# Performance work log

Measured on AMD Instinct MI355X. Metric: run time of the kernel, lower is better.

## Reference

```python
import jax, jax.numpy as jnp
import numpy as np

NODE_IN, EDGE_IN, HID, L = 16, 8, 128, 4
N_NODES, N_EDGES = 50000, 600000
EPS = 1e-5


def setup_inputs() -> dict:
    key = jax.random.key(0)
    ks = jax.random.split(key, 20)
    def lin(k, fan_in, fan_out):
        b = 1.0 / np.sqrt(fan_in)
        kw, kb = jax.random.split(k)
        return (jax.random.uniform(kw, (fan_in, fan_out), jnp.float32, -b, b),
                jax.random.uniform(kb, (fan_out,), jnp.float32, -b, b))
    x = jax.random.normal(ks[0], (N_NODES, NODE_IN), jnp.float32)
    edge_index = jax.random.randint(ks[1], (2, N_EDGES), 0, N_NODES, jnp.int64)
    edge_attr = jax.random.normal(ks[2], (N_EDGES, EDGE_IN), jnp.float32)
    node_w, node_b = lin(ks[3], NODE_IN, HID)
    edge_w, edge_b = lin(ks[4], EDGE_IN, HID)
    lnode_w, lnode_b, ledge_w, ledge_b, adm_w, adm_b = [], [], [], [], [], []
    for l in range(L):
        w, b = lin(ks[5 + 3 * l], HID, HID); lnode_w.append(w); lnode_b.append(b)
        w, b = lin(ks[6 + 3 * l], HID, HID); ledge_w.append(w); ledge_b.append(b)
        w, b = lin(ks[7 + 3 * l], HID, 1); adm_w.append(w); adm_b.append(b)
    return {
        "x": x, "edge_index": edge_index, "edge_attr": edge_attr,
        "node_w": node_w, "node_b": node_b, "edge_w": edge_w, "edge_b": edge_b,
        "lnode_w": jnp.stack(lnode_w), "lnode_b": jnp.stack(lnode_b),
        "ledge_w": jnp.stack(ledge_w), "ledge_b": jnp.stack(ledge_b),
        "adm_w": jnp.stack(adm_w), "adm_b": jnp.stack(adm_b),
        "gamma": jnp.ones((L, HID), jnp.float32),
        "beta": jnp.zeros((L, HID), jnp.float32),
    }


def reference(x, edge_index, edge_attr, node_w, node_b, edge_w, edge_b,
              lnode_w, lnode_b, ledge_w, ledge_b, adm_w, adm_b, gamma, beta):
    N = x.shape[0]
    src, dst = edge_index[0], edge_index[1]
    h = x @ node_w + node_b              # [N, HID]
    ea = edge_attr @ edge_w + edge_b     # [E, HID]
    for l in range(lnode_w.shape[0]):
        hn = h @ lnode_w[l] + lnode_b[l]                         # lin_node
        y_mag = jax.nn.sigmoid(ea @ adm_w[l] + adm_b[l])         # [E, 1] admittance gate
        e = ea @ ledge_w[l] + ledge_b[l]                         # lin_edge
        msg = y_mag * (hn[src] + e)                              # gated message [E, HID]
        agg = jax.ops.segment_sum(msg, dst, num_segments=N)      # scatter-add
        mu = jnp.mean(agg, axis=-1, keepdims=True)
        var = jnp.mean((agg - mu) ** 2, axis=-1, keepdims=True)
        xn = (agg - mu) * jax.lax.rsqrt(var + EPS) * gamma[l] + beta[l]
        h = h + jax.nn.relu(xn)          # dropout is identity in eval mode
    return h
```

## Files before the change

kernel.cpp:

```cpp
#include <hip/hip_runtime.h>
#include <math.h>

#define N_NODES 50000
#define N_EDGES 600000
#define HID 128
#define NLAYERS 4
#define NODE_IN 16
#define EDGE_IN 8
#define LN_EPS 1e-5f
#define SCAN_BLOCKS ((N_NODES + 255) / 256)
#define ENC_BASE (4864 + NLAYERS * HID * HID)
#define PRE_TOTAL (ENC_BASE + N_NODES * HID)

typedef short bf16x8 __attribute__((ext_vector_type(8)));
typedef float f32x4 __attribute__((ext_vector_type(4)));

__device__ __forceinline__ float b2f(unsigned short u) {
    union { unsigned int i; float f; } v; v.i = ((unsigned int)u) << 16; return v.f;
}
__device__ __forceinline__ unsigned short f2b(float x) {
    union { float f; unsigned int i; } v; v.f = x;
    unsigned int b = v.i + 0x7FFFu + ((v.i >> 16) & 1u);
    return (unsigned short)(b >> 16);
}

__global__ void detect_i64(const int* ei, int* flag) {
    __shared__ int nz;
    if (threadIdx.x == 0) nz = 0;
    __syncthreads();
    int acc = 0;
    for (int i = threadIdx.x; i < 1024; i += blockDim.x)
        if (ei[2 * i + 1] != 0) acc = 1;
    if (acc) atomicOr(&nz, 1);
    __syncthreads();
    if (threadIdx.x == 0) *flag = (nz == 0) ? 1 : 0;
}

__device__ __forceinline__ int edge_src(const void* ei, int f, int e) {
    if (f) return (int)((const long long*)ei)[e];
    return ((const int*)ei)[e];
}
__device__ __forceinline__ int edge_dst(const void* ei, int f, int e) {
    if (f) return (int)((const long long*)ei)[N_EDGES + e];
    return ((const int*)ei)[N_EDGES + e];
}

__global__ void hist_k(const void* ei, const int* flag, int* cursor) {
    int e = blockIdx.x * blockDim.x + threadIdx.x;
    if (e >= N_EDGES) return;
    int f = *flag;
    atomicAdd(&cursor[edge_dst(ei, f, e)], 1);
}

__global__ void scan1_k(const int* __restrict__ cursor, int* __restrict__ locex,
                        int* __restrict__ partials) {
    __shared__ int sd[256];
    int t = threadIdx.x, i = blockIdx.x * 256 + t;
    int v = (i < N_NODES) ? cursor[i] : 0;
    sd[t] = v;
    __syncthreads();
    for (int off = 1; off < 256; off <<= 1) {
        int x = (t >= off) ? sd[t - off] : 0;
        __syncthreads();
        sd[t] += x;
        __syncthreads();
    }
    if (i < N_NODES) locex[i] = sd[t] - v;
    if (t == 255) partials[blockIdx.x] = sd[255];
}

__global__ void scan2_k(int* partials) {
    __shared__ int sd[256];
    int t = threadIdx.x;
    int v = (t < SCAN_BLOCKS) ? partials[t] : 0;
    sd[t] = v;
    __syncthreads();
    for (int off = 1; off < 256; off <<= 1) {
        int x = (t >= off) ? sd[t - off] : 0;
        __syncthreads();
        sd[t] += x;
        __syncthreads();
    }
    if (t < SCAN_BLOCKS) partials[t] = sd[t] - v;
    if (t == 255) partials[SCAN_BLOCKS] = sd[255];
}

__global__ void scan3_k(int* __restrict__ row_ptr, int* __restrict__ cursor,
                        const int* __restrict__ partials) {
    int i = blockIdx.x * 256 + threadIdx.x;
    if (i < N_NODES) {
        int r = row_ptr[i] + partials[blockIdx.x];
        row_ptr[i] = r;
        cursor[i] = r;
    }
    if (i == N_NODES) row_ptr[N_NODES] = partials[SCAN_BLOCKS];
}

__global__ void place_k(const void* ei, const int* flag, int* cursor,
                        int* sorted_src, int* sorted_eid) {
    int e = blockIdx.x * blockDim.x + threadIdx.x;
    if (e >= N_EDGES) return;
    int f = *flag;
    int s = edge_src(ei, f, e);
    int d = edge_dst(ei, f, e);
    int pos = atomicAdd(&cursor[d], 1);
    sorted_src[pos] = s;
    sorted_eid[pos] = e;
}

__global__ void precomp_all_k(const float* __restrict__ edge_w, const float* __restrict__ edge_b,
                              const float* __restrict__ ledge_w, const float* __restrict__ ledge_b,
                              const float* __restrict__ lnode_b, const float* __restrict__ lnode_w,
                              const float* __restrict__ adm_w, const float* __restrict__ adm_b,
                              const float* __restrict__ x, const float* __restrict__ node_w,
                              const float* __restrict__ node_b,
                              float* __restrict__ M, float* __restrict__ cb,
                              float* __restrict__ v, float* __restrict__ cgate,
                              unsigned short* __restrict__ Wt16,
                              unsigned short* __restrict__ h16) {
    int t = blockIdx.x * 256 + threadIdx.x;
    if (t < 4096) {
        int l = t >> 10, k = (t >> 7) & 7, ch = t & 127;
        const float* lw = ledge_w + (size_t)l * HID * HID;
        float a = 0.f;
        for (int j = 0; j < HID; ++j) a += edge_w[k * HID + j] * lw[j * HID + ch];
        M[t] = a;
    } else if (t < 4608) {
        int u = t - 4096;
        int l = u >> 7, ch = u & 127;
        const float* lw = ledge_w + (size_t)l * HID * HID;
        float a = ledge_b[l * HID + ch] + lnode_b[l * HID + ch];
        for (int j = 0; j < HID; ++j) a += edge_b[j] * lw[j * HID + ch];
        cb[u] = a;
    } else if (t < 4640) {
        int u = t - 4608;
        int l = u >> 3, k = u & 7;
        float a = 0.f;
        for (int j = 0; j < HID; ++j) a += edge_w[k * HID + j] * adm_w[l * HID + j];
        v[u] = a;
    } else if (t < 4644) {
        int l = t - 4640;
        float a = adm_b[l];
        for (int j = 0; j < HID; ++j) a += edge_b[j] * adm_w[l * HID + j];
        cgate[l] = a;
    } else if (t >= 4864 && t < ENC_BASE) {
        int idx = t - 4864;
        int l = idx >> 14, r = idx & 16383, n = r >> 7, k = r & 127;
        Wt16[idx] = f2b(lnode_w[(size_t)l * HID * HID + k * HID + n]);
    } else if (t >= ENC_BASE && t < PRE_TOTAL) {
        int idx = t - ENC_BASE;
        int n = idx >> 7, c = idx & 127;
        float acc = node_b[c];
#pragma unroll
        for (int k = 0; k < NODE_IN; ++k) acc += x[n * NODE_IN + k] * node_w[k * HID + c];
        h16[idx] = f2b(acc);
    }
}

__global__ __launch_bounds__(256) void reorder_k(
    const int* __restrict__ sorted_eid, const float* __restrict__ edge_attr,
    const float* __restrict__ vw, const float* __restrict__ cgate,
    float* __restrict__ ea_sorted, float* __restrict__ y_sorted) {
    __shared__ float sv[36];
    if (threadIdx.x < 32) sv[threadIdx.x] = vw[threadIdx.x];
    else if (threadIdx.x < 36) sv[threadIdx.x] = cgate[threadIdx.x - 32];
    __syncthreads();
    int p = blockIdx.x * 256 + threadIdx.x;
    if (p >= N_EDGES) return;
    int eid = sorted_eid[p];
    float4 a0 = ((const float4*)edge_attr)[(size_t)eid * 2];
    float4 a1 = ((const float4*)edge_attr)[(size_t)eid * 2 + 1];
    ((float4*)ea_sorted)[(size_t)p * 2] = a0;
    ((float4*)ea_sorted)[(size_t)p * 2 + 1] = a1;
#pragma unroll
    for (int l = 0; l < NLAYERS; ++l) {
        const float* vl = &sv[l * 8];
        float t = sv[32 + l];
        t += a0.x * vl[0] + a0.y * vl[1] + a0.z * vl[2] + a0.w * vl[3];
        t += a1.x * vl[4] + a1.y * vl[5] + a1.z * vl[6] + a1.w * vl[7];
        y_sorted[(size_t)l * N_EDGES + p] = 1.0f / (1.0f + __expf(-t));
    }
}

__global__ __launch_bounds__(256) void node_stats_k(
    const int* __restrict__ row_ptr, const float* __restrict__ ea_sorted,
    const float* __restrict__ y_sorted,
    float* __restrict__ agg8, float* __restrict__ sy_arr) {
    int lane = threadIdx.x & 63;
    int n = (blockIdx.x * 256 + threadIdx.x) >> 6;
    int es = lane >> 3, k = lane & 7;
    int ps = row_ptr[n], pe = row_ptr[n + 1];
    float a0 = 0.f, a1 = 0.f, a2 = 0.f, a3 = 0.f;
    float s0 = 0.f, s1 = 0.f, s2 = 0.f, s3 = 0.f;
    for (int p = ps + es; p < pe; p += 8) {
        float ea = ea_sorted[(size_t)p * EDGE_IN + k];
        float y0 = y_sorted[(size_t)0 * N_EDGES + p];
        float y1 = y_sorted[(size_t)1 * N_EDGES + p];
        float y2 = y_sorted[(size_t)2 * N_EDGES + p];
        float y3 = y_sorted[(size_t)3 * N_EDGES + p];
        a0 += y0 * ea; a1 += y1 * ea; a2 += y2 * ea; a3 += y3 * ea;
        s0 += y0; s1 += y1; s2 += y2; s3 += y3;
    }
#pragma unroll
    for (int m = 8; m <= 32; m <<= 1) {
        a0 += __shfl_xor(a0, m, 64); a1 += __shfl_xor(a1, m, 64);
        a2 += __shfl_xor(a2, m, 64); a3 += __shfl_xor(a3, m, 64);
        s0 += __shfl_xor(s0, m, 64); s1 += __shfl_xor(s1, m, 64);
        s2 += __shfl_xor(s2, m, 64); s3 += __shfl_xor(s3, m, 64);
    }
    if (lane < 8) {
        agg8[((size_t)0 * N_NODES + n) * 8 + k] = a0;
        agg8[((size_t)1 * N_NODES + n) * 8 + k] = a1;
        agg8[((size_t)2 * N_NODES + n) * 8 + k] = a2;
        agg8[((size_t)3 * N_NODES + n) * 8 + k] = a3;
    }
    if (lane == 0) {
        sy_arr[(size_t)0 * N_NODES + n] = s0;
        sy_arr[(size_t)1 * N_NODES + n] = s1;
        sy_arr[(size_t)2 * N_NODES + n] = s2;
        sy_arr[(size_t)3 * N_NODES + n] = s3;
    }
}

__global__ __launch_bounds__(512, 4) void layer_fused_k(
    const int* __restrict__ row_ptr, const int* __restrict__ sorted_src,
    const float* __restrict__ y_l, const unsigned short* __restrict__ Wt16,
    const float* __restrict__ M_l, const float* __restrict__ cb_l,
    const float* __restrict__ agg8_l, const float* __restrict__ sy_l,
    const float* __restrict__ gm, const float* __restrict__ bt,
    const unsigned short* __restrict__ h16_in, unsigned short* __restrict__ h16_out,
    float* __restrict__ outF, int last) {
    __shared__ unsigned int ghs[16 * 66];
    __shared__ float red[8][16][2];
    const int wid = threadIdx.x >> 6, lane = threadIdx.x & 63;
    const int nbase = blockIdx.x * 16;

    {
        int rowA = wid * 2, rowB = wid * 2 + 1;
        int nA = nbase + rowA, nB = nbase + rowB;
        int pA = row_ptr[nA], eAe = row_ptr[nA + 1];
        int pB = row_ptr[nB], eBe = row_ptr[nB + 1];
        float aA0 = 0.f, aA1 = 0.f, aB0 = 0.f, aB1 = 0.f;

        while (pA + 3 < eAe && pB + 3 < eBe) {
            int sA[4], sB[4];
            float yA[4], yB[4];
            unsigned int vA[4], vB[4];
#pragma unroll
            for (int j = 0; j < 4; ++j) {
                sA[j] = sorted_src[pA + j]; yA[j] = y_l[pA + j];
                sB[j] = sorted_src[pB + j]; yB[j] = y_l[pB + j];
            }
#pragma unroll
            for (int j = 0; j < 4; ++j) {
                vA[j] = *(const unsigned int*)(h16_in + (size_t)sA[j] * HID + lane * 2);
                vB[j] = *(const unsigned int*)(h16_in + (size_t)sB[j] * HID + lane * 2);
            }
#pragma unroll
            for (int j = 0; j < 4; ++j) {
                aA0 += yA[j] * b2f((unsigned short)vA[j]);
                aA1 += yA[j] * b2f((unsigned short)(vA[j] >> 16));
                aB0 += yB[j] * b2f((unsigned short)vB[j]);
                aB1 += yB[j] * b2f((unsigned short)(vB[j] >> 16));
            }
            pA += 4; pB += 4;
        }
        for (; pA + 3 < eAe; pA += 4) {
            int s[4]; float y[4]; unsigned int v[4];
#pragma unroll
            for (int j = 0; j < 4; ++j) { s[j] = sorted_src[pA + j]; y[j] = y_l[pA + j]; }
#pragma unroll
            for (int j = 0; j < 4; ++j)
                v[j] = *(const unsigned int*)(h16_in + (size_t)s[j] * HID + lane * 2);
#pragma unroll
            for (int j = 0; j < 4; ++j) {
                aA0 += y[j] * b2f((unsigned short)v[j]);
                aA1 += y[j] * b2f((unsigned short)(v[j] >> 16));
            }
        }
        for (; pA < eAe; ++pA) {
            float y = y_l[pA];
            unsigned int v = *(const unsigned int*)(h16_in + (size_t)sorted_src[pA] * HID + lane * 2);
            aA0 += y * b2f((unsigned short)v);
            aA1 += y * b2f((unsigned short)(v >> 16));
        }
        for (; pB + 3 < eBe; pB += 4) {
            int s[4]; float y[4]; unsigned int v[4];
#pragma unroll
            for (int j = 0; j < 4; ++j) { s[j] = sorted_src[pB + j]; y[j] = y_l[pB + j]; }
#pragma unroll
            for (int j = 0; j < 4; ++j)
                v[j] = *(const unsigned int*)(h16_in + (size_t)s[j] * HID + lane * 2);
#pragma unroll
            for (int j = 0; j < 4; ++j) {
                aB0 += y[j] * b2f((unsigned short)v[j]);
                aB1 += y[j] * b2f((unsigned short)(v[j] >> 16));
            }
        }
        for (; pB < eBe; ++pB) {
            float y = y_l[pB];
            unsigned int v = *(const unsigned int*)(h16_in + (size_t)sorted_src[pB] * HID + lane * 2);
            aB0 += y * b2f((unsigned short)v);
            aB1 += y * b2f((unsigned short)(v >> 16));
        }
        ghs[rowA * 66 + lane] = ((unsigned int)f2b(aA1) << 16) | f2b(aA0);
        ghs[rowB * 66 + lane] = ((unsigned int)f2b(aB1) << 16) | f2b(aB0);
    }
    __syncthreads();

    const int g = lane >> 4, c = lane & 15;
    const int cf = wid;
    bf16x8 afrag[4];
#pragma unroll
    for (int kc = 0; kc < 4; ++kc) {
        union { unsigned int q[4]; bf16x8 v; } u;
        int base = c * 66 + kc * 16 + g * 4;
#pragma unroll
        for (int j = 0; j < 4; ++j) u.q[j] = ghs[base + j];
        afrag[kc] = u.v;
    }
    f32x4 acc = (f32x4){0.f, 0.f, 0.f, 0.f};
    {
        const unsigned short* wp = Wt16 + (size_t)(cf * 16 + c) * HID + g * 8;
#pragma unroll
        for (int kc = 0; kc < 4; ++kc) {
            bf16x8 bfrag = *(const bf16x8*)(wp + kc * 32);
            acc = __builtin_amdgcn_mfma_f32_16x16x32_bf16(afrag[kc], bfrag, acc, 0, 0, 0);
        }
    }

    const int ch = cf * 16 + c;
    float cbv = cb_l[ch], gav = gm[ch], bev = bt[ch];
    float mv[8];
#pragma unroll
    for (int k = 0; k < 8; ++k) mv[k] = M_l[k * HID + ch];
#pragma unroll
    for (int r = 0; r < 4; ++r) {
        int node = nbase + 4 * g + r;
        float sy = sy_l[node];
        float4 t0 = ((const float4*)agg8_l)[(size_t)node * 2];
        float4 t1 = ((const float4*)agg8_l)[(size_t)node * 2 + 1];
        float vv = sy * cbv;
        vv += t0.x * mv[0] + t0.y * mv[1] + t0.z * mv[2] + t0.w * mv[3];
        vv += t1.x * mv[4] + t1.y * mv[5] + t1.z * mv[6] + t1.w * mv[7];
        acc[r] += vv;
    }

    float sx[4], sq[4];
#pragma unroll
    for (int r = 0; r < 4; ++r) { sx[r] = acc[r]; sq[r] = acc[r] * acc[r]; }
#pragma unroll
    for (int m = 1; m <= 8; m <<= 1) {
#pragma unroll
        for (int r = 0; r < 4; ++r) {
            sx[r] += __shfl_xor(sx[r], m, 64);
            sq[r] += __shfl_xor(sq[r], m, 64);
        }
    }
    if (c == 0) {
#pragma unroll
        for (int r = 0; r < 4; ++r) {
            red[wid][4 * g + r][0] = sx[r];
            red[wid][4 * g + r][1] = sq[r];
        }
    }
    __syncthreads();

#pragma unroll
    for (int r = 0; r < 4; ++r) {
        int row = 4 * g + r;
        float SX = 0.f, SQ = 0.f;
#pragma unroll
        for (int w2 = 0; w2 < 8; ++w2) { SX += red[w2][row][0]; SQ += red[w2][row][1]; }
        float mean = SX * (1.0f / HID);
        float var = SQ * (1.0f / HID) - mean * mean;
        float rstd = rsqrtf(var + LN_EPS);
        int node = nbase + row;
        size_t idx = (size_t)node * HID + ch;
        float d = acc[r] - mean;
        float o = b2f(h16_in[idx]) + fmaxf(d * rstd * gav + bev, 0.f);
        if (last) outF[idx] = o;
        else      h16_out[idx] = f2b(o);
    }
}

extern "C" void kernel_launch(void* const* d_in, const int* in_sizes, int n_in,
                              void* d_out, int out_size, void* d_ws, size_t ws_size,
                              hipStream_t stream) {
    const float* x         = (const float*)d_in[0];
    const void*  ei        = d_in[1];
    const float* edge_attr = (const float*)d_in[2];
    const float* node_w    = (const float*)d_in[3];
    const float* node_b    = (const float*)d_in[4];
    const float* edge_w    = (const float*)d_in[5];
    const float* edge_b    = (const float*)d_in[6];
    const float* lnode_w   = (const float*)d_in[7];
    const float* lnode_b   = (const float*)d_in[8];
    const float* ledge_w   = (const float*)d_in[9];
    const float* ledge_b   = (const float*)d_in[10];
    const float* adm_w     = (const float*)d_in[11];
    const float* adm_b     = (const float*)d_in[12];
    const float* gamma     = (const float*)d_in[13];
    const float* beta      = (const float*)d_in[14];
    float* h = (float*)d_out;

    char* wp = (char*)d_ws;
    auto alloc = [&](size_t bytes) -> void* {
        void* p = (void*)wp;
        wp += (bytes + 255) & ~(size_t)255;
        return p;
    };
    int*            flag       = (int*)alloc(256);
    int*            cursor     = (int*)alloc(sizeof(int) * N_NODES);
    int*            row_ptr    = (int*)alloc(sizeof(int) * (N_NODES + 1));
    int*            partials   = (int*)alloc(sizeof(int) * (SCAN_BLOCKS + 1));
    int*            sorted_src = (int*)alloc(sizeof(int) * N_EDGES);
    int*            sorted_eid = (int*)alloc(sizeof(int) * N_EDGES);
    float*          ea_sorted  = (float*)alloc(sizeof(float) * (size_t)N_EDGES * EDGE_IN);
    float*          y_sorted   = (float*)alloc(sizeof(float) * NLAYERS * N_EDGES);
    float*          agg8       = (float*)alloc(sizeof(float) * NLAYERS * N_NODES * 8);
    float*          sy_arr     = (float*)alloc(sizeof(float) * NLAYERS * N_NODES);
    float*          Mw         = (float*)alloc(sizeof(float) * NLAYERS * 8 * HID);
    float*          cbw        = (float*)alloc(sizeof(float) * NLAYERS * HID);
    float*          vw         = (float*)alloc(sizeof(float) * NLAYERS * 8);
    float*          cgate      = (float*)alloc(sizeof(float) * NLAYERS);
    unsigned short* h16a       = (unsigned short*)alloc(sizeof(short) * (size_t)N_NODES * HID);
    unsigned short* h16b       = (unsigned short*)alloc(sizeof(short) * (size_t)N_NODES * HID);
    unsigned short* Wt16       = (unsigned short*)alloc(sizeof(short) * NLAYERS * HID * HID);
    (void)ws_size; (void)in_sizes; (void)n_in; (void)out_size;

    hipMemsetAsync(cursor, 0, sizeof(int) * N_NODES, stream);
    detect_i64<<<1, 256, 0, stream>>>((const int*)ei, flag);
    hist_k<<<(N_EDGES + 255) / 256, 256, 0, stream>>>(ei, flag, cursor);
    scan1_k<<<SCAN_BLOCKS, 256, 0, stream>>>(cursor, row_ptr, partials);
    scan2_k<<<1, 256, 0, stream>>>(partials);
    scan3_k<<<SCAN_BLOCKS, 256, 0, stream>>>(row_ptr, cursor, partials);
    place_k<<<(N_EDGES + 255) / 256, 256, 0, stream>>>(ei, flag, cursor, sorted_src, sorted_eid);
    precomp_all_k<<<(PRE_TOTAL + 255) / 256, 256, 0, stream>>>(
        edge_w, edge_b, ledge_w, ledge_b, lnode_b, lnode_w, adm_w, adm_b,
        x, node_w, node_b, Mw, cbw, vw, cgate, Wt16, h16a);
    reorder_k<<<(N_EDGES + 255) / 256, 256, 0, stream>>>(sorted_eid, edge_attr,
                                                         vw, cgate, ea_sorted, y_sorted);
    node_stats_k<<<N_NODES / 4, 256, 0, stream>>>(row_ptr, ea_sorted, y_sorted,
                                                  agg8, sy_arr);

    unsigned short* hin = h16a;
    unsigned short* hout = h16b;
    for (int l = 0; l < NLAYERS; ++l) {
        layer_fused_k<<<N_NODES / 16, 512, 0, stream>>>(
            row_ptr, sorted_src, y_sorted + (size_t)l * N_EDGES,
            Wt16 + (size_t)l * HID * HID,
            Mw + (size_t)l * 8 * HID, cbw + (size_t)l * HID,
            agg8 + (size_t)l * N_NODES * 8, sy_arr + (size_t)l * N_NODES,
            gamma + (size_t)l * HID, beta + (size_t)l * HID,
            hin, hout, h, (l == NLAYERS - 1) ? 1 : 0);
        unsigned short* t = hin; hin = hout; hout = t;
    }
}
```

Measured before the change: 357.8 us.

## Sort nodes by in-degree to balance per-tile gather work in layer kernel

Builds a counting sort of nodes by in-degree (histogram in scan3, a scan kernel, and a placement kernel), ordering nodes from highest to lowest degree. The fused layer kernel then processes 16-node tiles taken from this permutation instead of contiguous node ranges. Warps in a tile, which pair up nodes, now see similar edge counts, which reduces divergence and idle waves, and heavy tiles are scheduled first. In exchange, node-feature, agg8, sy and output accesses become scattered rather than contiguous, and preprocessing gains two extra kernel launches plus atomics.

```diff
diff --git a/kernel.cpp b/kernel.cpp
--- a/kernel.cpp
+++ b/kernel.cpp
@@ -24,9 +24,10 @@
     return (unsigned short)(b >> 16);
 }
 
-__global__ void detect_i64(const int* ei, int* flag) {
+__global__ void detect_i64(const int* ei, int* flag, int* dhist) {
     __shared__ int nz;
     if (threadIdx.x == 0) nz = 0;
+    dhist[threadIdx.x] = 0;
     __syncthreads();
     int acc = 0;
     for (int i = threadIdx.x; i < 1024; i += blockDim.x)
@@ -86,14 +87,41 @@
 }
 
 __global__ void scan3_k(int* __restrict__ row_ptr, int* __restrict__ cursor,
-                        const int* __restrict__ partials) {
+                        const int* __restrict__ partials, int* __restrict__ dhist) {
     int i = blockIdx.x * 256 + threadIdx.x;
     if (i < N_NODES) {
+        int d = cursor[i];
         int r = row_ptr[i] + partials[blockIdx.x];
         row_ptr[i] = r;
         cursor[i] = r;
+        atomicAdd(&dhist[d > 255 ? 255 : d], 1);
     }
     if (i == N_NODES) row_ptr[N_NODES] = partials[SCAN_BLOCKS];
+}
+
+__global__ void dscan_k(const int* __restrict__ dhist, int* __restrict__ dcur) {
+    __shared__ int sd[256];
+    int t = threadIdx.x;
+    int v = dhist[t];
+    sd[t] = v;
+    __syncthreads();
+    for (int off = 1; off < 256; off <<= 1) {
+        int x = (t >= off) ? sd[t - off] : 0;
+        __syncthreads();
+        sd[t] += x;
+        __syncthreads();
+    }
+    dcur[t] = sd[t] - v;
+}
+
+__global__ void dplace_k(const int* __restrict__ row_ptr, int* __restrict__ dcur,
+                         int* __restrict__ nodes_by_deg) {
+    int n = blockIdx.x * 256 + threadIdx.x;
+    if (n >= N_NODES) return;
+    int d = row_ptr[n + 1] - row_ptr[n];
+    if (d > 255) d = 255;
+    int pos = atomicAdd(&dcur[d], 1);
+    nodes_by_deg[N_NODES - 1 - pos] = n;
 }
 
 __global__ void place_k(const void* ei, const int* flag, int* cursor,
@@ -223,6 +251,7 @@
 }
 
 __global__ __launch_bounds__(512, 4) void layer_fused_k(
+    const int* __restrict__ nodes_by_deg,
     const int* __restrict__ row_ptr, const int* __restrict__ sorted_src,
     const float* __restrict__ y_l, const unsigned short* __restrict__ Wt16,
     const float* __restrict__ M_l, const float* __restrict__ cb_l,
@@ -232,12 +261,15 @@
     float* __restrict__ outF, int last) {
     __shared__ unsigned int ghs[16 * 66];
     __shared__ float red[8][16][2];
+    __shared__ int tile_nodes[16];
     const int wid = threadIdx.x >> 6, lane = threadIdx.x & 63;
-    const int nbase = blockIdx.x * 16;
+    const int tbase = blockIdx.x * 16;
+    if (threadIdx.x < 16) tile_nodes[threadIdx.x] = nodes_by_deg[tbase + threadIdx.x];
+    __syncthreads();
 
     {
         int rowA = wid * 2, rowB = wid * 2 + 1;
-        int nA = nbase + rowA, nB = nbase + rowB;
+        int nA = tile_nodes[rowA], nB = tile_nodes[rowB];
         int pA = row_ptr[nA], eAe = row_ptr[nA + 1];
         int pB = row_ptr[nB], eBe = row_ptr[nB + 1];
         float aA0 = 0.f, aA1 = 0.f, aB0 = 0.f, aB1 = 0.f;
@@ -336,7 +368,7 @@
     for (int k = 0; k < 8; ++k) mv[k] = M_l[k * HID + ch];
 #pragma unroll
     for (int r = 0; r < 4; ++r) {
-        int node = nbase + 4 * g + r;
+        int node = tile_nodes[4 * g + r];
         float sy = sy_l[node];
         float4 t0 = ((const float4*)agg8_l)[(size_t)node * 2];
         float4 t1 = ((const float4*)agg8_l)[(size_t)node * 2 + 1];
@@ -375,7 +407,7 @@
         float mean = SX * (1.0f / HID);
         float var = SQ * (1.0f / HID) - mean * mean;
         float rstd = rsqrtf(var + LN_EPS);
-        int node = nbase + row;
+        int node = tile_nodes[row];
         size_t idx = (size_t)node * HID + ch;
         float d = acc[r] - mean;
         float o = b2f(h16_in[idx]) + fmaxf(d * rstd * gav + bev, 0.f);
@@ -414,6 +446,9 @@
     int*            cursor     = (int*)alloc(sizeof(int) * N_NODES);
     int*            row_ptr    = (int*)alloc(sizeof(int) * (N_NODES + 1));
     int*            partials   = (int*)alloc(sizeof(int) * (SCAN_BLOCKS + 1));
+    int*            dhist      = (int*)alloc(sizeof(int) * 256);
+    int*            dcur       = (int*)alloc(sizeof(int) * 256);
+    int*            nodes_bd   = (int*)alloc(sizeof(int) * N_NODES);
     int*            sorted_src = (int*)alloc(sizeof(int) * N_EDGES);
     int*            sorted_eid = (int*)alloc(sizeof(int) * N_EDGES);
     float*          ea_sorted  = (float*)alloc(sizeof(float) * (size_t)N_EDGES * EDGE_IN);
@@ -430,11 +465,13 @@
     (void)ws_size; (void)in_sizes; (void)n_in; (void)out_size;
 
     hipMemsetAsync(cursor, 0, sizeof(int) * N_NODES, stream);
-    detect_i64<<<1, 256, 0, stream>>>((const int*)ei, flag);
+    detect_i64<<<1, 256, 0, stream>>>((const int*)ei, flag, dhist);
     hist_k<<<(N_EDGES + 255) / 256, 256, 0, stream>>>(ei, flag, cursor);
     scan1_k<<<SCAN_BLOCKS, 256, 0, stream>>>(cursor, row_ptr, partials);
     scan2_k<<<1, 256, 0, stream>>>(partials);
-    scan3_k<<<SCAN_BLOCKS, 256, 0, stream>>>(row_ptr, cursor, partials);
+    scan3_k<<<SCAN_BLOCKS, 256, 0, stream>>>(row_ptr, cursor, partials, dhist);
+    dscan_k<<<1, 256, 0, stream>>>(dhist, dcur);
+    dplace_k<<<SCAN_BLOCKS, 256, 0, stream>>>(row_ptr, dcur, nodes_bd);
     place_k<<<(N_EDGES + 255) / 256, 256, 0, stream>>>(ei, flag, cursor, sorted_src, sorted_eid);
     precomp_all_k<<<(PRE_TOTAL + 255) / 256, 256, 0, stream>>>(
         edge_w, edge_b, ledge_w, ledge_b, lnode_b, lnode_w, adm_w, adm_b,
@@ -448,7 +485,7 @@
     unsigned short* hout = h16b;
     for (int l = 0; l < NLAYERS; ++l) {
         layer_fused_k<<<N_NODES / 16, 512, 0, stream>>>(
-            row_ptr, sorted_src, y_sorted + (size_t)l * N_EDGES,
+            nodes_bd, row_ptr, sorted_src, y_sorted + (size_t)l * N_EDGES,
             Wt16 + (size_t)l * HID * HID,
             Mw + (size_t)l * 8 * HID, cbw + (size_t)l * HID,
             agg8 + (size_t)l * N_NODES * 8, sy_arr + (size_t)l * N_NODES,
```

Result: slower. 694.9 us (+94.2%).
